# Kernel optimization log

Measured on AMD Instinct MI355X. Metric: run time of the kernel, lower is better.

## Reference

```python
import jax, jax.numpy as jnp
import numpy as np

BETA = 0.25
COMMIT_W = 1.0
EPS = 1e-6
N_E, E_DIM, C = 8192, 256, 256
B, H, W = 16, 32, 32


def setup_inputs() -> dict:
    key = jax.random.key(0)
    k1, k2, k3 = jax.random.split(key, 3)
    z = jax.random.normal(k1, (B, C, H, W), jnp.float32)
    frozen_codebook = jax.random.normal(k2, (N_E, E_DIM), jnp.float32) * (E_DIM ** -0.5)
    w_transform = jax.random.normal(k3, (C, E_DIM), jnp.float32) * (E_DIM ** -0.5)
    return {"z": z, "frozen_codebook": frozen_codebook, "w_transform": w_transform}


def _rotate_to(src, tgt):
    # Rotation trick: Householder-style rotation of src onto direction of tgt.
    sg = jax.lax.stop_gradient
    norm_src = jnp.linalg.norm(src, axis=-1, keepdims=True)
    norm_tgt = jnp.linalg.norm(tgt, axis=-1, keepdims=True)
    u = src / jnp.clip(norm_src, EPS)          # normalized source
    q = tgt / jnp.clip(norm_tgt, EPS)          # normalized target
    w = u + q
    w = sg(w / jnp.clip(jnp.linalg.norm(w, axis=-1, keepdims=True), EPS))
    u = sg(u)
    q = sg(q)
    e = src  # gradients flow through e only (rotation matrix is detached)
    rotated = (e
               - 2.0 * jnp.sum(e * w, axis=-1, keepdims=True) * w
               + 2.0 * jnp.sum(e * u, axis=-1, keepdims=True) * q)
    return rotated * sg(norm_tgt / jnp.clip(norm_src, EPS))


def reference(z, frozen_codebook, w_transform):
    z = z.astype(jnp.float32)
    zc = jnp.transpose(z, (0, 2, 3, 1))          # b h w c
    z_flat = zc.reshape(-1, zc.shape[-1])        # [N, C]
    codebook = frozen_codebook @ w_transform.T   # [n_e, C] (Linear, no bias)

    # squared L2 distances, argmin under no_grad
    d = (jnp.sum(z_flat ** 2, axis=1, keepdims=True)
         + jnp.sum(codebook ** 2, axis=1)
         - 2.0 * jnp.einsum('bd,nd->bn', z_flat, codebook))
    indices = jnp.argmin(jax.lax.stop_gradient(d), axis=1)  # [N]

    z_q_flat = codebook[indices]                 # [N, C]
    sg = jax.lax.stop_gradient
    loss = (jnp.mean((sg(z_flat) - z_q_flat) ** 2)
            + BETA * jnp.mean((z_flat - sg(z_q_flat)) ** 2)) * COMMIT_W

    z_q_flat = _rotate_to(z_flat, z_q_flat)      # rotation trick
    z_q = z_q_flat.reshape(zc.shape)             # b h w c
    z_q = jnp.transpose(z_q, (0, 3, 1, 2))       # b c h w
    return z_q, loss, indices
```

## Files before the change

### kernel.cpp

```cpp
#include <hip/hip_runtime.h>
#include <math.h>

typedef unsigned short u16;
typedef unsigned int   u32;

#define B_   16
#define C_   256
#define HW_  1024
#define N_   16384
#define NE_  8192
#define K_   256
#define NSPLIT 4
#define CPS  2048
#define NZQ  4194304

typedef _Float16 f16x8 __attribute__((ext_vector_type(8)));
typedef float    f32x16 __attribute__((ext_vector_type(16)));


__device__ __forceinline__ u16 f2h(float x) {
    union { _Float16 h; u16 u; } c;
    c.h = (_Float16)x;
    return c.u;
}

__global__ void k_transpose_z(const float* __restrict__ z, float* __restrict__ zf,
                              u16* __restrict__ zh) {
    __shared__ float tile[32][33];
    int b   = blockIdx.z;
    int hw0 = blockIdx.x * 32;
    int c0  = blockIdx.y * 32;
    int tx = threadIdx.x;
    int ty = threadIdx.y;
    #pragma unroll
    for (int i = 0; i < 4; ++i) {
        int c = c0 + ty + i * 8;
        tile[ty + i * 8][tx] = z[((size_t)b * C_ + c) * HW_ + hw0 + tx];
    }
    __syncthreads();
    #pragma unroll
    for (int i = 0; i < 4; ++i) {
        int hw = hw0 + ty + i * 8;
        size_t o = ((size_t)b * HW_ + hw) * C_ + c0 + tx;
        float v = tile[tx][ty + i * 8];
        zf[o] = v;
        zh[o] = f2h(v);
    }
}

__global__ __launch_bounds__(256) void k_codebook_gemm(
        const float* __restrict__ f, const float* __restrict__ w,
        float* __restrict__ cb, u16* __restrict__ cbh) {
    __shared__ float Fs[16][68];
    __shared__ float Ws[16][68];
    int n0 = blockIdx.x * 64;
    int c0 = blockIdx.y * 64;
    int tid = threadIdx.x;
    int tx = tid & 15, ty = tid >> 4;
    int nl = tid >> 2;
    int kq = (tid & 3) * 4;
    float acc[4][4] = {};
    float4 fv = *(const float4*)&f[(size_t)(n0 + nl) * K_ + kq];
    float4 wv = *(const float4*)&w[(size_t)(c0 + nl) * K_ + kq];
    for (int kb = 0; kb < K_; kb += 16) {
        __syncthreads();
        Fs[kq + 0][nl] = fv.x; Fs[kq + 1][nl] = fv.y; Fs[kq + 2][nl] = fv.z; Fs[kq + 3][nl] = fv.w;
        Ws[kq + 0][nl] = wv.x; Ws[kq + 1][nl] = wv.y; Ws[kq + 2][nl] = wv.z; Ws[kq + 3][nl] = wv.w;
        __syncthreads();
        if (kb + 16 < K_) {
            fv = *(const float4*)&f[(size_t)(n0 + nl) * K_ + kb + 16 + kq];
            wv = *(const float4*)&w[(size_t)(c0 + nl) * K_ + kb + 16 + kq];
        }
        #pragma unroll
        for (int k = 0; k < 16; ++k) {
            float4 a = *(float4*)&Fs[k][ty * 4];
            float4 b = *(float4*)&Ws[k][tx * 4];
            float av[4] = {a.x, a.y, a.z, a.w};
            float bv[4] = {b.x, b.y, b.z, b.w};
            #pragma unroll
            for (int i = 0; i < 4; ++i)
                #pragma unroll
                for (int j = 0; j < 4; ++j)
                    acc[i][j] += av[i] * bv[j];
        }
    }
    #pragma unroll
    for (int i = 0; i < 4; ++i) {
        size_t o = (size_t)(n0 + ty * 4 + i) * K_ + c0 + tx * 4;
        *(float4*)&cb[o] = make_float4(acc[i][0], acc[i][1], acc[i][2], acc[i][3]);
        *(ushort4*)&cbh[o] = make_ushort4(f2h(acc[i][0]), f2h(acc[i][1]),
                                          f2h(acc[i][2]), f2h(acc[i][3]));
    }
}

__global__ void k_c2(const float* __restrict__ cb, float* __restrict__ c2,
                     double* __restrict__ c2d) {
    int row  = blockIdx.x * 4 + (threadIdx.x >> 6);
    int lane = threadIdx.x & 63;
    float4 v = *(const float4*)&cb[(size_t)row * K_ + lane * 4];
    double s = (double)v.x * v.x + (double)v.y * v.y
             + (double)v.z * v.z + (double)v.w * v.w;
    #pragma unroll
    for (int off = 32; off; off >>= 1) s += __shfl_down(s, off, 64);
    if (lane == 0) { c2d[row] = s; c2[row] = (float)(s * 4096.0 + 262144.0); }
}

__device__ __forceinline__ void ld_lds16(const void* g, void* l) {
    __builtin_amdgcn_global_load_lds((const __attribute__((address_space(1))) void*)g,
                                     (__attribute__((address_space(3))) void*)l, 16, 0, 0);
}

#define INS(M1, M2, U) { u32 t_ = min(M1, U); u32 h_ = max(M1, U); M1 = t_; M2 = min(M2, h_); }

#define SCORE16(ACC, M1, M2, CGBASE, C2B) do {                                    \
    u32 ib_ = (u32)(code0 + (CGBASE));                                            \
    _Pragma("unroll")                                                             \
    for (int h = 0; h < 4; ++h) {                                                 \
        float4 cv = *(const float4*)&(C2B)[(CGBASE) + 8 * h];                     \
        u32 u0 = (((u32)fmaf(-8192.f, (ACC)[4*h+0], cv.x)) << 13) + ib_ + 8*h + 0; \
        u32 u1 = (((u32)fmaf(-8192.f, (ACC)[4*h+1], cv.y)) << 13) + ib_ + 8*h + 1; \
        u32 u2 = (((u32)fmaf(-8192.f, (ACC)[4*h+2], cv.z)) << 13) + ib_ + 8*h + 2; \
        u32 u3 = (((u32)fmaf(-8192.f, (ACC)[4*h+3], cv.w)) << 13) + ib_ + 8*h + 3; \
        INS(M1, M2, u0); INS(M1, M2, u1); INS(M1, M2, u2); INS(M1, M2, u3);       \
    }                                                                             \
} while (0)

#define WAITVM(N) { asm volatile("s_waitcnt vmcnt(" #N ")" ::: "memory"); \
                    __builtin_amdgcn_s_barrier();                          \
                    __builtin_amdgcn_sched_barrier(0); }

__global__ __launch_bounds__(256, 2) void k_scan_mfma(
        const u16* __restrict__ zh, const u16* __restrict__ cbh,
        const float* __restrict__ c2, int* __restrict__ t2i) {
    __shared__ __align__(16) u16 sA[4][8192];
    __shared__ __align__(16) float c2s[2048];

    int r0    = blockIdx.x * 128;
    int split = blockIdx.y;
    int tid  = threadIdx.x;
    int wave = tid >> 6, lane = tid & 63;
    int l31 = lane & 31, q = lane >> 5;
    int ra = ((wave & 1) << 6) + l31;

    const u16* zp = zh + (size_t)(r0 + ((wave >> 1) << 6) + l31) * K_ + q * 8;
    f16x8 zr0[16], zr1[16];
    #pragma unroll
    for (int t = 0; t < 16; ++t) {
        zr0[t] = *(const f16x8*)&zp[t * 16];
        zr1[t] = *(const f16x8*)&zp[32 * K_ + t * 16];
    }

    size_t ga[4]; u32 la[4];
    #pragma unroll
    for (int it = 0; it < 4; ++it) {
        int S = (it * 4 + wave) * 64 + lane;
        int row = S >> 3, u = S & 7;
        ga[it] = (size_t)row * K_ + (u ^ (row & 7)) * 8;
        la[it] = (u32)(it * 4 + wave) * 512;
    }

    u32 m1a = 0xFFFFFFFFu, m2a = 0xFFFFFFFFu;
    u32 m1b = 0xFFFFFFFFu, m2b = 0xFFFFFFFFu;

    const u16* cb0 = cbh + (size_t)split * CPS * K_;

    auto STAGE = [&](int s) {
        const u16* Ab = cb0 + (size_t)(s >> 2) * (128 * K_) + (s & 3) * 64;
        u16* d = &sA[s & 3][0];
        #pragma unroll
        for (int it = 0; it < 4; ++it) ld_lds16(Ab + ga[it], d + la[it]);
    };

    f32x16 acc0 = (f32x16){}, acc1 = (f32x16){}, acc2 = (f32x16){}, acc3 = (f32x16){};

    auto COMPUTE = [&](int ct, int kb) {
        const u16* sAb = &sA[kb][0];
        __builtin_amdgcn_s_setprio(1);
        #pragma unroll
        for (int ks = 0; ks < 4; ++ks) {
            u32 u8 = (u32)(((ks * 2 + q) ^ (l31 & 7)) * 8);
            f16x8 af0 = *(const f16x8*)&sAb[(u32)ra * 64 + u8];
            f16x8 af1 = *(const f16x8*)&sAb[(u32)ra * 64 + 2048 + u8];
            acc0 = __builtin_amdgcn_mfma_f32_32x32x16_f16(af0, zr0[kb * 4 + ks], acc0, 0, 0, 0);
            acc1 = __builtin_amdgcn_mfma_f32_32x32x16_f16(af1, zr0[kb * 4 + ks], acc1, 0, 0, 0);
            acc2 = __builtin_amdgcn_mfma_f32_32x32x16_f16(af0, zr1[kb * 4 + ks], acc2, 0, 0, 0);
            acc3 = __builtin_amdgcn_mfma_f32_32x32x16_f16(af1, zr1[kb * 4 + ks], acc3, 0, 0, 0);
        }
        __builtin_amdgcn_s_setprio(0);
        if (kb == 3) {
            int code0 = split * CPS + ct * 128;
            const float* C2B = &c2s[ct * 128];
            int cga = ((wave & 1) << 6) + (q << 2);
            int cgb = cga + 32;
            SCORE16(acc0, m1a, m2a, cga, C2B);
            SCORE16(acc1, m1a, m2a, cgb, C2B);
            SCORE16(acc2, m1b, m2b, cga, C2B);
            SCORE16(acc3, m1b, m2b, cgb, C2B);
            acc0 = (f32x16){}; acc1 = (f32x16){}; acc2 = (f32x16){}; acc3 = (f32x16){};
        }
    };

    STAGE(0); STAGE(1);
    ld_lds16(&c2[split * CPS + wave * 512 + lane * 4], &c2s[wave * 512]);
    ld_lds16(&c2[split * CPS + wave * 512 + 256 + lane * 4], &c2s[wave * 512 + 256]);
    asm volatile("s_waitcnt vmcnt(0)" ::: "memory");
    __builtin_amdgcn_s_barrier();
    __builtin_amdgcn_sched_barrier(0);

    for (int ct = 0; ct < 15; ++ct) {
        #pragma unroll
        for (int kb = 0; kb < 4; ++kb) {
            STAGE(ct * 4 + kb + 2);
            WAITVM(8);
            COMPUTE(ct, kb);
        }
    }
    STAGE(62); WAITVM(8); COMPUTE(15, 0);
    STAGE(63); WAITVM(8); COMPUTE(15, 1);
    WAITVM(4);            COMPUTE(15, 2);
    WAITVM(0);            COMPUTE(15, 3);

    {
        u32 o1 = __shfl_xor(m1a, 32, 64), o2 = __shfl_xor(m2a, 32, 64);
        u32 h = max(m1a, o1); m1a = min(m1a, o1); m2a = min(min(m2a, o2), h);
        o1 = __shfl_xor(m1b, 32, 64); o2 = __shfl_xor(m2b, 32, 64);
        h = max(m1b, o1); m1b = min(m1b, o1); m2b = min(min(m2b, o2), h);
    }
    u32* mbuf = (u32*)&sA[0][0];
    if (q == 0) {
        int base = ((wave * 2 + 0) * 32 + l31) * 2;
        mbuf[base] = m1a; mbuf[base + 1] = m2a;
        base = ((wave * 2 + 1) * 32 + l31) * 2;
        mbuf[base] = m1b; mbuf[base + 1] = m2b;
    }
    __syncthreads();
    if (tid < 128) {
        int zr = tid, wp = zr >> 6, zg = (zr >> 5) & 1, l = zr & 31;
        int iA = (((wp * 2 + 0) * 2 + zg) * 32 + l) * 2;
        int iB = (((wp * 2 + 1) * 2 + zg) * 32 + l) * 2;
        u32 a1 = mbuf[iA], a2 = mbuf[iA + 1];
        u32 b1 = mbuf[iB], b2 = mbuf[iB + 1];
        u32 h  = max(a1, b1), f1 = min(a1, b1);
        u32 f2 = min(min(a2, b2), h);
        size_t o = ((size_t)split * N_ + (r0 + zr)) * 2;
        t2i[o] = (int)f1;
        t2i[o + 1] = (int)f2;
    }
}

__global__ __launch_bounds__(256) void k_finalize(
        const float* __restrict__ zf, const float* __restrict__ cb,
        const double* __restrict__ c2d, const u32* __restrict__ t2i,
        float* __restrict__ out) {
    __shared__ int   bidx[16];
    __shared__ float wsum[4];
    __shared__ float tile[16][260];
    int n0 = blockIdx.x * 16;
    int tid = threadIdx.x;
    int wv = tid >> 6, lane = tid & 63;
    int h = lane >> 5, l5 = lane & 31;
    const u32 W = 160u << 13;

    for (int rr = 0; rr < 4; ++rr) {
        int n = n0 + wv * 4 + rr;
        u32 pk[4];
        u32 b1 = 0xFFFFFFFFu, b2 = 0xFFFFFFFFu;
        #pragma unroll
        for (int p = 0; p < 4; ++p) {
            u32 pa = t2i[((size_t)p * N_ + n) * 2 + 0];
            u32 pb = t2i[((size_t)p * N_ + n) * 2 + 1];
            pk[p] = h ? pb : pa;
            INS(b1, b2, pa); INS(b1, b2, pb);
        }

        int bi;
        if (b2 - b1 >= W) {
            bi = (int)(b1 & 0x1FFFu);
        } else {
            const float* zp = zf + (size_t)n * K_;
            float4 za = *(const float4*)&zp[l5 * 4];
            float4 zb = *(const float4*)&zp[l5 * 4 + 128];
            int cid[4];
            #pragma unroll
            for (int p = 0; p < 4; ++p) cid[p] = (int)(pk[p] & 0x1FFFu);
            double c2p[4];
            #pragma unroll
            for (int p = 0; p < 4; ++p) c2p[p] = c2d[cid[p]];
            float4 cva = *(const float4*)&cb[(size_t)cid[0] * K_ + l5 * 4];
            float4 cvb = *(const float4*)&cb[(size_t)cid[0] * K_ + l5 * 4 + 128];

            double bs = 1e300; bi = 0x7fffffff;
            #pragma unroll
            for (int p = 0; p < 4; ++p) {
                float4 ca = cva, cbv = cvb;
                if (p < 3) {
                    cva = *(const float4*)&cb[(size_t)cid[p + 1] * K_ + l5 * 4];
                    cvb = *(const float4*)&cb[(size_t)cid[p + 1] * K_ + l5 * 4 + 128];
                }
                double acc = (double)za.x * ca.x + (double)za.y * ca.y
                           + (double)za.z * ca.z + (double)za.w * ca.w
                           + (double)zb.x * cbv.x + (double)zb.y * cbv.y
                           + (double)zb.z * cbv.z + (double)zb.w * cbv.w;
                #pragma unroll
                for (int off = 1; off < 32; off <<= 1) acc += __shfl_xor(acc, off, 32);
                double sc = c2p[p] - 2.0 * acc;
                int    ci = cid[p];
                double so = __shfl_xor(sc, 32, 64);
                int    io = __shfl_xor(ci, 32, 64);
                double s0 = h ? so : sc;  int i0 = h ? io : ci;
                double s1 = h ? sc : so;  int i1 = h ? ci : io;
                if (s0 < bs || (s0 == bs && i0 < bi)) { bs = s0; bi = i0; }
                if (s1 < bs || (s1 == bs && i1 < bi)) { bs = s1; bi = i1; }
            }
        }
        if (lane == 0) {
            bidx[wv * 4 + rr] = bi;
            out[(size_t)NZQ + 1 + n] = (float)bi;
        }
    }
    __syncthreads();

    float accl = 0.f;
    for (int l = 0; l < 16; ++l) {
        int n = n0 + l;
        int bi = bidx[l];
        float zq = cb[(size_t)bi * K_ + tid];
        float d  = zf[(size_t)n * K_ + tid] - zq;
        accl += d * d;
        tile[l][tid] = zq;
    }
    #pragma unroll
    for (int off = 32; off; off >>= 1) accl += __shfl_down(accl, off, 64);
    if ((tid & 63) == 0) wsum[tid >> 6] = accl;
    __syncthreads();
    if (tid == 0)
        atomicAdd(out + NZQ, (wsum[0] + wsum[1] + wsum[2] + wsum[3]) * (1.25f / (float)NZQ));
    int b = n0 >> 10, hw0 = n0 & 1023;
    #pragma unroll
    for (int g = 0; g < 4; ++g) {
        float4 v = make_float4(tile[g * 4 + 0][tid], tile[g * 4 + 1][tid],
                               tile[g * 4 + 2][tid], tile[g * 4 + 3][tid]);
        *(float4*)&out[((size_t)b * C_ + tid) * HW_ + hw0 + g * 4] = v;
    }
}

extern "C" void kernel_launch(void* const* d_in, const int* in_sizes, int n_in,
                              void* d_out, int out_size, void* d_ws, size_t ws_size,
                              hipStream_t stream) {
    const float* z  = (const float*)d_in[0];
    const float* fc = (const float*)d_in[1];
    const float* wt = (const float*)d_in[2];
    float* out = (float*)d_out;

    float* ws = (float*)d_ws;
    const size_t OFF_ZF   = 0;
    const size_t OFF_CB   = OFF_ZF + (size_t)N_ * K_;
    const size_t OFF_C2   = OFF_CB + (size_t)NE_ * K_;
    const size_t OFF_C2D  = OFF_C2 + NE_;
    const size_t OFF_T2I  = OFF_C2D + (size_t)NE_ * 2;
    const size_t OFF_ZH   = OFF_T2I + (size_t)NSPLIT * N_ * 2;
    const size_t OFF_CBH  = OFF_ZH + (size_t)N_ * K_ / 2;

    float*  zf   = ws + OFF_ZF;
    float*  cb   = ws + OFF_CB;
    float*  c2   = ws + OFF_C2;
    double* c2d  = (double*)(ws + OFF_C2D);
    int*    t2i  = (int*)(ws + OFF_T2I);
    u16*    zh   = (u16*)(ws + OFF_ZH);
    u16*    cbh  = (u16*)(ws + OFF_CBH);

    k_transpose_z<<<dim3(HW_ / 32, C_ / 32, B_), dim3(32, 8), 0, stream>>>(z, zf, zh);
    k_codebook_gemm<<<dim3(NE_ / 64, K_ / 64), 256, 0, stream>>>(fc, wt, cb, cbh);
    k_c2<<<NE_ / 4, 256, 0, stream>>>(cb, c2, c2d);
    k_scan_mfma<<<dim3(N_ / 128, NSPLIT), 256, 0, stream>>>(zh, cbh, c2, t2i);
    k_finalize<<<N_ / 16, 256, 0, stream>>>(zf, cb, c2d, (const u32*)t2i, out);
}
```

Measured before the change: 198.0 us.

## Merge transpose, codebook GEMM and norm kernels into one launch

Combines the z transpose and the codebook GEMM into a single kernel whose block index selects the role. The separate codebook-norm kernel is replaced by per-tile partial sums of squares written from the GEMM epilogue, and the scan kernel adds those partials itself when filling its shared norm table. This removes two kernel launches and the extra pass over the codebook, at the cost of redundant partial-sum reads in every scan block and a synchronous prologue in place of the async LDS load.

Result: no change. 197.4 us (-0.3%).

```diff
diff --git a/kernel.cpp b/kernel.cpp
--- a/kernel.cpp
+++ b/kernel.cpp
@@ -24,38 +24,43 @@
     return c.u;
 }
 
-__global__ void k_transpose_z(const float* __restrict__ z, float* __restrict__ zf,
-                              u16* __restrict__ zh) {
-    __shared__ float tile[32][33];
-    int b   = blockIdx.z;
-    int hw0 = blockIdx.x * 32;
-    int c0  = blockIdx.y * 32;
-    int tx = threadIdx.x;
-    int ty = threadIdx.y;
-    #pragma unroll
-    for (int i = 0; i < 4; ++i) {
-        int c = c0 + ty + i * 8;
-        tile[ty + i * 8][tx] = z[((size_t)b * C_ + c) * HW_ + hw0 + tx];
-    }
-    __syncthreads();
-    #pragma unroll
-    for (int i = 0; i < 4; ++i) {
-        int hw = hw0 + ty + i * 8;
-        size_t o = ((size_t)b * HW_ + hw) * C_ + c0 + tx;
-        float v = tile[tx][ty + i * 8];
-        zf[o] = v;
-        zh[o] = f2h(v);
-    }
-}
-
-__global__ __launch_bounds__(256) void k_codebook_gemm(
-        const float* __restrict__ f, const float* __restrict__ w,
-        float* __restrict__ cb, u16* __restrict__ cbh) {
+__global__ __launch_bounds__(256) void k_pre(
+        const float* __restrict__ z, const float* __restrict__ f,
+        const float* __restrict__ w, float* __restrict__ zf,
+        u16* __restrict__ zh, float* __restrict__ cb, u16* __restrict__ cbh,
+        double* __restrict__ c2part) {
+    __shared__ float tileT[32][33];
     __shared__ float Fs[16][68];
     __shared__ float Ws[16][68];
-    int n0 = blockIdx.x * 64;
-    int c0 = blockIdx.y * 64;
+    int bid = blockIdx.x;
     int tid = threadIdx.x;
+
+    if (bid >= 512) {
+        int b2  = bid - 512;
+        int hw0 = (b2 & 31) * 32;
+        int c0  = ((b2 >> 5) & 7) * 32;
+        int b   = b2 >> 8;
+        int tx = tid & 31;
+        int ty = tid >> 5;
+        #pragma unroll
+        for (int i = 0; i < 4; ++i) {
+            int c = c0 + ty + i * 8;
+            tileT[ty + i * 8][tx] = z[((size_t)b * C_ + c) * HW_ + hw0 + tx];
+        }
+        __syncthreads();
+        #pragma unroll
+        for (int i = 0; i < 4; ++i) {
+            int hw = hw0 + ty + i * 8;
+            size_t o = ((size_t)b * HW_ + hw) * C_ + c0 + tx;
+            float v = tileT[tx][ty + i * 8];
+            zf[o] = v;
+            zh[o] = f2h(v);
+        }
+        return;
+    }
+
+    int n0 = (bid & 127) * 64;
+    int c0 = (bid >> 7) * 64;
     int tx = tid & 15, ty = tid >> 4;
     int nl = tid >> 2;
     int kq = (tid & 3) * 4;
@@ -90,19 +95,12 @@
         *(float4*)&cb[o] = make_float4(acc[i][0], acc[i][1], acc[i][2], acc[i][3]);
         *(ushort4*)&cbh[o] = make_ushort4(f2h(acc[i][0]), f2h(acc[i][1]),
                                           f2h(acc[i][2]), f2h(acc[i][3]));
-    }
-}
-
-__global__ void k_c2(const float* __restrict__ cb, float* __restrict__ c2,
-                     double* __restrict__ c2d) {
-    int row  = blockIdx.x * 4 + (threadIdx.x >> 6);
-    int lane = threadIdx.x & 63;
-    float4 v = *(const float4*)&cb[(size_t)row * K_ + lane * 4];
-    double s = (double)v.x * v.x + (double)v.y * v.y
-             + (double)v.z * v.z + (double)v.w * v.w;
-    #pragma unroll
-    for (int off = 32; off; off >>= 1) s += __shfl_down(s, off, 64);
-    if (lane == 0) { c2d[row] = s; c2[row] = (float)(s * 4096.0 + 262144.0); }
+        double ps = (double)acc[i][0] * acc[i][0] + (double)acc[i][1] * acc[i][1]
+                  + (double)acc[i][2] * acc[i][2] + (double)acc[i][3] * acc[i][3];
+        #pragma unroll
+        for (int off = 8; off; off >>= 1) ps += __shfl_down(ps, off, 16);
+        if (tx == 0) c2part[(size_t)(n0 + ty * 4 + i) * 4 + (c0 >> 6)] = ps;
+    }
 }
 
 __device__ __forceinline__ void ld_lds16(const void* g, void* l) {
@@ -131,7 +129,8 @@
 
 __global__ __launch_bounds__(256, 2) void k_scan_mfma(
         const u16* __restrict__ zh, const u16* __restrict__ cbh,
-        const float* __restrict__ c2, int* __restrict__ t2i) {
+        const double* __restrict__ c2part, double* __restrict__ c2d,
+        int* __restrict__ t2i) {
     __shared__ __align__(16) u16 sA[4][8192];
     __shared__ __align__(16) float c2s[2048];
 
@@ -200,11 +199,19 @@
         }
     };
 
+    {
+        const double* cp = c2part + (size_t)split * CPS * 4;
+        #pragma unroll
+        for (int r = 0; r < 8; ++r) {
+            int row = tid * 8 + r;
+            const double* pr = cp + (size_t)row * 4;
+            double s = (pr[0] + pr[1]) + (pr[2] + pr[3]);
+            c2s[row] = (float)(s * 4096.0 + 262144.0);
+            if (blockIdx.x == 0) c2d[split * CPS + row] = s;
+        }
+    }
     STAGE(0); STAGE(1);
-    ld_lds16(&c2[split * CPS + wave * 512 + lane * 4], &c2s[wave * 512]);
-    ld_lds16(&c2[split * CPS + wave * 512 + 256 + lane * 4], &c2s[wave * 512 + 256]);
-    asm volatile("s_waitcnt vmcnt(0)" ::: "memory");
-    __builtin_amdgcn_s_barrier();
+    __syncthreads();
     __builtin_amdgcn_sched_barrier(0);
 
     for (int ct = 0; ct < 15; ++ct) {
@@ -355,23 +362,21 @@
     float* ws = (float*)d_ws;
     const size_t OFF_ZF   = 0;
     const size_t OFF_CB   = OFF_ZF + (size_t)N_ * K_;
-    const size_t OFF_C2   = OFF_CB + (size_t)NE_ * K_;
-    const size_t OFF_C2D  = OFF_C2 + NE_;
+    const size_t OFF_C2P  = OFF_CB + (size_t)NE_ * K_;
+    const size_t OFF_C2D  = OFF_C2P + (size_t)NE_ * 8;
     const size_t OFF_T2I  = OFF_C2D + (size_t)NE_ * 2;
     const size_t OFF_ZH   = OFF_T2I + (size_t)NSPLIT * N_ * 2;
     const size_t OFF_CBH  = OFF_ZH + (size_t)N_ * K_ / 2;
 
-    float*  zf   = ws + OFF_ZF;
-    float*  cb   = ws + OFF_CB;
-    float*  c2   = ws + OFF_C2;
-    double* c2d  = (double*)(ws + OFF_C2D);
-    int*    t2i  = (int*)(ws + OFF_T2I);
-    u16*    zh   = (u16*)(ws + OFF_ZH);
-    u16*    cbh  = (u16*)(ws + OFF_CBH);
-
-    k_transpose_z<<<dim3(HW_ / 32, C_ / 32, B_), dim3(32, 8), 0, stream>>>(z, zf, zh);
-    k_codebook_gemm<<<dim3(NE_ / 64, K_ / 64), 256, 0, stream>>>(fc, wt, cb, cbh);
-    k_c2<<<NE_ / 4, 256, 0, stream>>>(cb, c2, c2d);
-    k_scan_mfma<<<dim3(N_ / 128, NSPLIT), 256, 0, stream>>>(zh, cbh, c2, t2i);
+    float*  zf     = ws + OFF_ZF;
+    float*  cb     = ws + OFF_CB;
+    double* c2part = (double*)(ws + OFF_C2P);
+    double* c2d    = (double*)(ws + OFF_C2D);
+    int*    t2i    = (int*)(ws + OFF_T2I);
+    u16*    zh     = (u16*)(ws + OFF_ZH);
+    u16*    cbh    = (u16*)(ws + OFF_CBH);
+
+    k_pre<<<4608, 256, 0, stream>>>(z, fc, wt, zf, zh, cb, cbh, c2part);
+    k_scan_mfma<<<dim3(N_ / 128, NSPLIT), 256, 0, stream>>>(zh, cbh, c2part, c2d, t2i);
     k_finalize<<<N_ / 16, 256, 0, stream>>>(zf, cb, c2d, (const u32*)t2i, out);
 }
```
